# Performance work log

Hardware: AMD Instinct MI355X
Metric: run time of the kernel (lower is better)

Reference implementation:

```python
import jax, jax.numpy as jnp
import numpy as np

H_OUT, W_OUT = 473, 473  # original image size the logits are upsampled to
BN_EPS = 1e-5


def _conv(x, w, pad):
    return jax.lax.conv_general_dilated(
        x, w, window_strides=(1, 1), padding=[(pad, pad), (pad, pad)],
        dimension_numbers=('NCHW', 'OIHW', 'NCHW'))


def _bn(x, g, b):
    # BatchNorm2d in training mode: batch statistics over (N, H, W)
    m = jnp.mean(x, axis=(0, 2, 3), keepdims=True)
    v = jnp.var(x, axis=(0, 2, 3), keepdims=True)
    return (x - m) * jax.lax.rsqrt(v + BN_EPS) * g.reshape(1, -1, 1, 1) + b.reshape(1, -1, 1, 1)


def setup_inputs() -> dict:
    key = jax.random.key(0)
    ks = jax.random.split(key, 8)
    B, C, Hf, Wf, NC = 2, 256, 60, 60, 2
    return {
        'V_a': jax.random.normal(ks[0], (B, C, Hf, Wf), jnp.float32),
        'V_b': jax.random.normal(ks[1], (B, C, Hf, Wf), jnp.float32),
        'D_a': jax.random.normal(ks[2], (B, C, Hf, Wf), jnp.float32),
        'W_e': jax.random.normal(ks[3], (C, C), jnp.float32) * 0.02,
        'gate_w': jax.random.normal(ks[4], (1, C, 1, 1), jnp.float32) * 0.01,
        'conv1_w': jax.random.normal(ks[5], (C, 3 * C, 3, 3), jnp.float32) * 0.01,
        'conv2_w': jax.random.normal(ks[6], (C, 2 * C, 3, 3), jnp.float32) * 0.01,
        'bn1_g': jnp.ones((C,), jnp.float32),
        'bn1_b': jnp.zeros((C,), jnp.float32),
        'bn2_g': jnp.ones((C,), jnp.float32),
        'bn2_b': jnp.zeros((C,), jnp.float32),
        'cls1_w': jax.random.normal(ks[7], (NC, C, 1, 1), jnp.float32) * 0.01,
        'cls1_b': jnp.zeros((NC,), jnp.float32),
        'cls2_w': jax.random.normal(jax.random.fold_in(key, 9), (NC, C, 1, 1), jnp.float32) * 0.01,
        'cls2_b': jnp.zeros((NC,), jnp.float32),
    }


def reference(V_a, V_b, D_a, W_e, gate_w, conv1_w, conv2_w,
              bn1_g, bn1_b, bn2_g, bn2_b, cls1_w, cls1_b, cls2_w, cls2_b):
    B, C, Hf, Wf = V_a.shape
    N = Hf * Wf
    V_a_flat = V_a.reshape(B, C, N)
    V_b_flat = V_b.reshape(B, C, N)

    # linear_e on transposed A features, then affinity S = (A^T W^T) B
    weighted = jnp.einsum('bcn,dc->bnd', V_a_flat, W_e)        # [B, N, C]
    S = jnp.einsum('bnd,bdm->bnm', weighted, V_b_flat)         # [B, N, N]

    S_row = jax.nn.softmax(S, axis=1)                          # softmax over dim 1
    S_colT = jax.nn.softmax(jnp.swapaxes(S, 1, 2), axis=1)     # softmax of S^T over dim 1

    Z_b = jnp.einsum('bcn,bnm->bcm', V_a_flat, S_row)          # attended for view b
    Z_a = jnp.einsum('bcn,bnm->bcm', V_b_flat, S_colT)         # attended for view a

    att1 = Z_a.reshape(B, C, Hf, Wf)
    att2 = Z_b.reshape(B, C, Hf, Wf)

    # 1x1 sigmoid gates
    att1 = att1 * jax.nn.sigmoid(_conv(att1, gate_w, 0))
    att2 = att2 * jax.nn.sigmoid(_conv(att2, gate_w, 0))

    # conc1: branch-1 concatenates gated attention, RGB feat, and depth feat
    x1 = jnp.concatenate([att1, V_a, D_a], axis=1)             # [B, 3C, Hf, Wf]
    x2 = jnp.concatenate([att2, V_b], axis=1)                  # [B, 2C, Hf, Wf]

    x1 = jax.nn.relu(_bn(_conv(x1, conv1_w, 1), bn1_g, bn1_b))
    x2 = jax.nn.relu(_bn(_conv(x2, conv2_w, 1), bn2_g, bn2_b))

    x1 = _conv(x1, cls1_w, 0) + cls1_b.reshape(1, -1, 1, 1)
    x2 = _conv(x2, cls2_w, 0) + cls2_b.reshape(1, -1, 1, 1)

    NC = cls1_w.shape[0]
    x1 = jax.image.resize(x1, (B, NC, H_OUT, W_OUT), 'linear')
    x2 = jax.image.resize(x2, (B, NC, H_OUT, W_OUT), 'linear')
    return jax.nn.sigmoid(x1), jax.nn.sigmoid(x2)
```

## Files before the change

kernel.cpp:

```cpp
#include <hip/hip_runtime.h>

#define BB 2
#define CC 256
#define NN 3600
#define NCH 2
#define HO 473
#define WO 473
#define NP 3648
#define NR 3712
#define NTI 29
#define ZKS 6
#define CZKS 3

typedef unsigned short u16;
typedef __attribute__((ext_vector_type(8))) short short8;
typedef __attribute__((ext_vector_type(4))) float f32x4;

static __device__ __forceinline__ u16 f2bf(float f) {
    unsigned u = __float_as_uint(f);
    unsigned r = (u + 0x7FFF + ((u >> 16) & 1)) >> 16;
    return (u16)r;
}
static __device__ __forceinline__ u16 f2h(float f) {
    _Float16 h = (_Float16)f;
    return __builtin_bit_cast(unsigned short, h);
}
static __device__ __forceinline__ float h2f(u16 u) {
    _Float16 h = __builtin_bit_cast(_Float16, u);
    return (float)h;
}

static __device__ __forceinline__ void glds16(const u16* g, u16* l) {
    __builtin_amdgcn_global_load_lds(
        (const __attribute__((address_space(1))) void*)g,
        (__attribute__((address_space(3))) void*)l, 16, 0, 0);
}


__global__ __launch_bounds__(256)
void gemm_we(const u16* __restrict__ vat, const u16* __restrict__ web,
             u16* __restrict__ wgtb)
{
    __shared__ u16 As[128 * 64];
    __shared__ u16 Bs[128 * 64];
    const u16* A = vat + (long)blockIdx.z * NR * CC;
    u16* Cp = wgtb + (long)blockIdx.z * NR * CC;

    const int t = threadIdx.x;
    const int w = t >> 6, lane = t & 63;
    const int mh = (w >> 1) * 64, nh = (w & 1) * 64;
    const int lm = lane & 15, quad = lane >> 4;
    const int m0 = blockIdx.y * 128, n0 = blockIdx.x * 128;
    const int wb = t & 192;

    f32x4 acc[4][4] = {};

    for (int k0 = 0; k0 < CC; k0 += 64) {
#pragma unroll
        for (int i = 0; i < 4; ++i) {
            int idx = i * 256 + t;
            int row = idx >> 3;
            int sc8 = ((idx ^ row) & 7) * 8;
            glds16(A + (long)(m0 + row) * CC + k0 + sc8, &As[(i * 256 + wb) * 8]);
            glds16(web + (long)(n0 + row) * CC + k0 + sc8, &Bs[(i * 256 + wb) * 8]);
        }
        __syncthreads();
#pragma unroll
        for (int s = 0; s < 2; ++s) {
            short8 a[4], b[4];
#pragma unroll
            for (int i = 0; i < 4; ++i)
                a[i] = *(const short8*)(&As[(mh + i * 16 + lm) * 64 + ((s * 4 + quad) ^ (lm & 7)) * 8]);
#pragma unroll
            for (int j = 0; j < 4; ++j)
                b[j] = *(const short8*)(&Bs[(nh + j * 16 + lm) * 64 + ((s * 4 + quad) ^ (lm & 7)) * 8]);
#pragma unroll
            for (int i = 0; i < 4; ++i)
#pragma unroll
                for (int j = 0; j < 4; ++j)
                    acc[i][j] = __builtin_amdgcn_mfma_f32_16x16x32_bf16(a[i], b[j], acc[i][j], 0, 0, 0);
        }
        __syncthreads();
    }
#pragma unroll
    for (int i = 0; i < 4; ++i)
#pragma unroll
        for (int r = 0; r < 4; ++r) {
            int row = m0 + mh + i * 16 + quad * 4 + r;
            if (row < NN)
#pragma unroll
                for (int j = 0; j < 4; ++j) {
                    int col = n0 + nh + j * 16 + lm;
                    if (col < CC) Cp[(long)row * CC + col] = f2bf(acc[i][j][r]);
                }
        }
}

__global__ __launch_bounds__(256)
void gemm_s_stats(const u16* __restrict__ A, const u16* __restrict__ B,
                  u16* __restrict__ Sh, u16* __restrict__ STh,
                  float* __restrict__ prowm, float* __restrict__ prows,
                  float* __restrict__ pcolm, float* __restrict__ pcols)
{
    __shared__ u16 smem[17408];
    u16* As = smem;
    u16* Bs = smem + 8192;

    const int t = threadIdx.x;
    const int w = t >> 6, lane = t & 63;
    const int mh = (w >> 1) * 64, nh = (w & 1) * 64;
    const int lm = lane & 15, quad = lane >> 4;
    const int m0 = blockIdx.y * 128, n0 = blockIdx.x * 128;
    const int wb = t & 192;

    f32x4 acc[4][4] = {};

    for (int k0 = 0; k0 < CC; k0 += 64) {
#pragma unroll
        for (int i = 0; i < 4; ++i) {
            int idx = i * 256 + t;
            int row = idx >> 3;
            int sc8 = ((idx ^ row) & 7) * 8;
            glds16(A + (long)(m0 + row) * CC + k0 + sc8, &As[(i * 256 + wb) * 8]);
            glds16(B + (long)(n0 + row) * CC + k0 + sc8, &Bs[(i * 256 + wb) * 8]);
        }
        __syncthreads();
#pragma unroll
        for (int s = 0; s < 2; ++s) {
            short8 a[4], b[4];
#pragma unroll
            for (int i = 0; i < 4; ++i)
                a[i] = *(const short8*)(&As[(mh + i * 16 + lm) * 64 + ((s * 4 + quad) ^ (lm & 7)) * 8]);
#pragma unroll
            for (int j = 0; j < 4; ++j)
                b[j] = *(const short8*)(&Bs[(nh + j * 16 + lm) * 64 + ((s * 4 + quad) ^ (lm & 7)) * 8]);
#pragma unroll
            for (int i = 0; i < 4; ++i)
#pragma unroll
                for (int j = 0; j < 4; ++j)
                    acc[i][j] = __builtin_amdgcn_mfma_f32_16x16x32_bf16(a[i], b[j], acc[i][j], 0, 0, 0);
        }
        __syncthreads();
    }

#pragma unroll
    for (int i = 0; i < 4; ++i)
#pragma unroll
        for (int r = 0; r < 4; ++r) {
            int row = m0 + mh + i * 16 + quad * 4 + r;
            if (row < NN)
#pragma unroll
                for (int j = 0; j < 4; ++j) {
                    int col = n0 + nh + j * 16 + lm;
                    if (col < NN) Sh[(long)row * NP + col] = f2h(acc[i][j][r]);
                }
        }

    bool cval[4];
#pragma unroll
    for (int j = 0; j < 4; ++j) cval[j] = (n0 + nh + j * 16 + lm) < NN;

    float* sm = (float*)smem;
    float* rowm = sm;
    float* rows_ = sm + 256;
    float* colm = sm + 512;
    float* cols_ = sm + 768;
    __syncthreads();

#pragma unroll
    for (int i = 0; i < 4; ++i)
#pragma unroll
        for (int r = 0; r < 4; ++r) {
            float m = -3.0e38f;
#pragma unroll
            for (int j = 0; j < 4; ++j) if (cval[j]) m = fmaxf(m, acc[i][j][r]);
            m = fmaxf(m, __shfl_xor(m, 1, 64));
            m = fmaxf(m, __shfl_xor(m, 2, 64));
            m = fmaxf(m, __shfl_xor(m, 4, 64));
            m = fmaxf(m, __shfl_xor(m, 8, 64));
            float s = 0.f;
#pragma unroll
            for (int j = 0; j < 4; ++j) if (cval[j]) s += __expf(acc[i][j][r] - m);
            s += __shfl_xor(s, 1, 64);
            s += __shfl_xor(s, 2, 64);
            s += __shfl_xor(s, 4, 64);
            s += __shfl_xor(s, 8, 64);
            if (lm == 0) {
                int rr = mh + i * 16 + quad * 4 + r;
                rowm[(w & 1) * 128 + rr] = m;
                rows_[(w & 1) * 128 + rr] = s;
            }
        }

#pragma unroll
    for (int j = 0; j < 4; ++j) {
        float m = -3.0e38f;
#pragma unroll
        for (int i = 0; i < 4; ++i)
#pragma unroll
            for (int r = 0; r < 4; ++r)
                if (m0 + mh + i * 16 + quad * 4 + r < NN) m = fmaxf(m, acc[i][j][r]);
        m = fmaxf(m, __shfl_xor(m, 16, 64));
        m = fmaxf(m, __shfl_xor(m, 32, 64));
        float s = 0.f;
#pragma unroll
        for (int i = 0; i < 4; ++i)
#pragma unroll
            for (int r = 0; r < 4; ++r)
                if (m0 + mh + i * 16 + quad * 4 + r < NN) s += __expf(acc[i][j][r] - m);
        s += __shfl_xor(s, 16, 64);
        s += __shfl_xor(s, 32, 64);
        if (quad == 0) {
            int ccl = nh + j * 16 + lm;
            colm[(w >> 1) * 128 + ccl] = m;
            cols_[(w >> 1) * 128 + ccl] = s;
        }
    }
    __syncthreads();

    if (t < 128) {
        float m1 = rowm[t], m2 = rowm[128 + t];
        float M = fmaxf(m1, m2);
        float s = rows_[t] * __expf(m1 - M) + rows_[128 + t] * __expf(m2 - M);
        if (m0 + t < NN) {
            prowm[(long)blockIdx.x * NR + m0 + t] = M;
            prows[(long)blockIdx.x * NR + m0 + t] = s;
        }
    } else {
        int c = t - 128;
        float m1 = colm[c], m2 = colm[128 + c];
        float M = fmaxf(m1, m2);
        float s = cols_[c] * __expf(m1 - M) + cols_[128 + c] * __expf(m2 - M);
        if (n0 + c < NN) {
            pcolm[(long)blockIdx.y * NR + n0 + c] = M;
            pcols[(long)blockIdx.y * NR + n0 + c] = s;
        }
    }

    __syncthreads();
    u16* tr = smem;
#pragma unroll
    for (int i = 0; i < 4; ++i)
#pragma unroll
        for (int j = 0; j < 4; ++j)
#pragma unroll
            for (int r = 0; r < 4; ++r)
                tr[(nh + j * 16 + lm) * 136 + (mh + i * 16 + quad * 4 + r)] = f2h(acc[i][j][r]);
    __syncthreads();
    {
        int row = t >> 1, hf = t & 1;
        int mg = n0 + row;
        if (mg < NN) {
#pragma unroll
            for (int q = 0; q < 8; ++q) {
                int cb = m0 + hf * 64 + q * 8;
                if (cb < NN)
                    *(uint4*)(&STh[(long)mg * NP + cb]) =
                        *(const uint4*)(&tr[row * 136 + hf * 64 + q * 8]);
            }
        }
    }
}

__global__ __launch_bounds__(256)
void stats_combine(const float* __restrict__ prowm, const float* __restrict__ prows,
                   const float* __restrict__ pcolm, const float* __restrict__ pcols,
                   float* __restrict__ rmx, float* __restrict__ rsm,
                   float* __restrict__ cmx, float* __restrict__ csm)
{
    int i = blockIdx.x * 256 + threadIdx.x;
    if (i >= NN) return;
    const float* pm = blockIdx.y ? pcolm : prowm;
    const float* ps = blockIdx.y ? pcols : prows;
    float m = -3.0e38f, s = 0.f;
#pragma unroll 4
    for (int tI = 0; tI < NTI; ++tI) {
        float m2 = pm[(long)tI * NR + i], s2 = ps[(long)tI * NR + i];
        float M = fmaxf(m, m2);
        s = s * __expf(m - M) + s2 * __expf(m2 - M);
        m = M;
    }
    if (blockIdx.y) { cmx[i] = m; csm[i] = s; }
    else            { rmx[i] = m; rsm[i] = s; }
}

__global__ __launch_bounds__(256)
void p_build(u16* __restrict__ Sh, u16* __restrict__ STh,
             const float* __restrict__ rmx, const float* __restrict__ rsm,
             const float* __restrict__ cmx, const float* __restrict__ csm)
{
    int r = blockIdx.x;
    u16* M = blockIdx.y ? STh : Sh;
    const float* mx = blockIdx.y ? cmx : rmx;
    const float* sm = blockIdx.y ? csm : rsm;
    float mv = mx[r];
    float inv = 1.f / sm[r];
    u16* row = M + (long)r * NP;
    int t = threadIdx.x;
    for (int c0 = t * 8; c0 < NP; c0 += 2048) {
        uint4 hv = *(const uint4*)(row + c0);
        const u16* hp = (const u16*)&hv;
        u16 o[8];
#pragma unroll
        for (int e = 0; e < 8; ++e) {
            int c = c0 + e;
            o[e] = (c < NN) ? f2bf(__expf(h2f(hp[e]) - mv) * inv) : (u16)0;
        }
        *(uint4*)(row + c0) = *(const uint4*)o;
    }
}

__global__ __launch_bounds__(256, 4)
void gemm_z_128(const u16* __restrict__ vab_b, const u16* __restrict__ vbb_b,
                const u16* __restrict__ PT, const u16* __restrict__ P,
                float* __restrict__ Zb_b, float* __restrict__ Za_b)
{
    __shared__ u16 As[128 * 64];
    __shared__ u16 Bs[128 * 64];

    const int t = threadIdx.x;
    const int w = t >> 6, lane = t & 63;
    const int mh = (w >> 1) * 64, nh = (w & 1) * 64;
    const int lm = lane & 15, quad = lane >> 4;
    const int n0 = blockIdx.x * 128;
    const int ks = blockIdx.y;
    const int zz = blockIdx.z;
    const int branch = zz & 1;
    const int m0 = (zz >> 1) * 128;
    const u16* A = branch ? vbb_b : vab_b;
    const u16* B = branch ? P : PT;
    float* Cp = branch ? Za_b : Zb_b;
    const int wb = t & 192;

    const int base = 57 / ZKS, rem = 57 % ZKS;
    const int it0 = ks * base + (ks < rem ? ks : rem);
    const int itn = base + (ks < rem ? 1 : 0);

    f32x4 acc[4][4] = {};

    for (int it = it0; it < it0 + itn; ++it) {
        const int k0 = it * 64;
#pragma unroll
        for (int i = 0; i < 4; ++i) {
            int idx = i * 256 + t;
            int row = idx >> 3;
            int sc8 = ((idx ^ row) & 7) * 8;
            glds16(A + (long)(m0 + row) * NP + k0 + sc8, &As[(i * 256 + wb) * 8]);
            glds16(B + (long)(n0 + row) * NP + k0 + sc8, &Bs[(i * 256 + wb) * 8]);
        }
        __syncthreads();
#pragma unroll
        for (int s = 0; s < 2; ++s) {
            short8 a[4], b[4];
#pragma unroll
            for (int i = 0; i < 4; ++i)
                a[i] = *(const short8*)(&As[(mh + i * 16 + lm) * 64 + ((s * 4 + quad) ^ (lm & 7)) * 8]);
#pragma unroll
            for (int j = 0; j < 4; ++j)
                b[j] = *(const short8*)(&Bs[(nh + j * 16 + lm) * 64 + ((s * 4 + quad) ^ (lm & 7)) * 8]);
#pragma unroll
            for (int i = 0; i < 4; ++i)
#pragma unroll
                for (int j = 0; j < 4; ++j)
                    acc[i][j] = __builtin_amdgcn_mfma_f32_16x16x32_bf16(a[i], b[j], acc[i][j], 0, 0, 0);
        }
        __syncthreads();
    }

#pragma unroll
    for (int i = 0; i < 4; ++i)
#pragma unroll
        for (int r = 0; r < 4; ++r) {
            int row = m0 + mh + i * 16 + quad * 4 + r;
#pragma unroll
            for (int j = 0; j < 4; ++j) {
                int col = n0 + nh + j * 16 + lm;
                if (col < NN)
                    atomicAdd(&Cp[(long)row * NN + col], acc[i][j][r]);
            }
        }
}

__global__ __launch_bounds__(256, 4)
void conv_both(const u16* __restrict__ W1, const u16* __restrict__ W2,
               const u16* __restrict__ gzaT, const u16* __restrict__ vat,
               const u16* __restrict__ daT, const u16* __restrict__ gzbT,
               const u16* __restrict__ vbt, const u16* __restrict__ zbuf,
               float* __restrict__ y1, float* __restrict__ y2)
{
    __shared__ u16 As[128 * 64];
    __shared__ u16 Bs[128 * 64];

    const int t = threadIdx.x;
    const int w = t >> 6, lane = t & 63;
    const int mh = (w >> 1) * 64, nh = (w & 1) * 64;
    const int lm = lane & 15, quad = lane >> 4;
    const int wb = t & 192;

    const long L = blockIdx.x + (long)NTI * (blockIdx.y + (long)CZKS * blockIdx.z);
    const int combo = (int)(L & 7);
    const long rest = L >> 3;
    const int ks = (int)(rest % CZKS);
    const int px = (int)(rest / CZKS);
    const int which = combo >> 2;
    const int b = (combo >> 1) & 1;
    const int m0 = (combo & 1) * 128;
    const int n0 = px * 128;

    const int CIN = which ? 512 : 768;
    const int KT = 9 * CIN;
    const u16* W = which ? W2 : W1;
    const u16* P0 = which ? gzbT : gzaT;
    const u16* P1 = which ? vbt : vat;
    const u16* P2 = which ? vbt : daT;
    float* Y = which ? y2 : y1;
    const long pstride = (long)NR * CC;

    const int per = (KT / 64) / CZKS;
    const int it0 = ks * per;

    int pv[4], hv[4], wv[4], sc8v[4];
#pragma unroll
    for (int i = 0; i < 4; ++i) {
        int idx = i * 256 + t;
        int row = idx >> 3;
        sc8v[i] = ((idx ^ row) & 7) * 8;
        pv[i] = n0 + row;
        hv[i] = pv[i] / 60;
        wv[i] = pv[i] - hv[i] * 60;
    }

    f32x4 acc[4][4] = {};

    for (int it = it0; it < it0 + per; ++it) {
        const int k0 = it * 64;
        int tap = k0 / CIN;
        int kloc = k0 - tap * CIN;
        int plane = kloc >> 8, cip = kloc & 255;
        int dh = tap / 3 - 1, dw = tap - (tap / 3) * 3 - 1;
        int off = dh * 60 + dw;
        const u16* src = (plane == 0) ? P0 : ((plane == 1) ? P1 : P2);
        src += (long)b * pstride + cip;

#pragma unroll
        for (int i = 0; i < 4; ++i) {
            int idx = i * 256 + t;
            int row = idx >> 3;
            glds16(W + (long)(m0 + row) * KT + k0 + sc8v[i], &As[(i * 256 + wb) * 8]);
            bool ok = pv[i] < NN && (unsigned)(hv[i] + dh) < 60u && (unsigned)(wv[i] + dw) < 60u;
            const u16* gs = ok ? src + (long)(pv[i] + off) * CC + sc8v[i] : zbuf;
            glds16(gs, &Bs[(i * 256 + wb) * 8]);
        }
        __syncthreads();
#pragma unroll
        for (int s = 0; s < 2; ++s) {
            short8 a[4], bfr[4];
#pragma unroll
            for (int i = 0; i < 4; ++i)
                a[i] = *(const short8*)(&As[(mh + i * 16 + lm) * 64 + ((s * 4 + quad) ^ (lm & 7)) * 8]);
#pragma unroll
            for (int j = 0; j < 4; ++j)
                bfr[j] = *(const short8*)(&Bs[(nh + j * 16 + lm) * 64 + ((s * 4 + quad) ^ (lm & 7)) * 8]);
#pragma unroll
            for (int i = 0; i < 4; ++i)
#pragma unroll
                for (int j = 0; j < 4; ++j)
                    acc[i][j] = __builtin_amdgcn_mfma_f32_16x16x32_bf16(a[i], bfr[j], acc[i][j], 0, 0, 0);
        }
        __syncthreads();
    }

    float* out = Y + (long)b * CC * NN;
#pragma unroll
    for (int i = 0; i < 4; ++i)
#pragma unroll
        for (int r = 0; r < 4; ++r) {
            int row = m0 + mh + i * 16 + quad * 4 + r;
#pragma unroll
            for (int j = 0; j < 4; ++j) {
                int col = n0 + nh + j * 16 + lm;
                if (col < NN)
                    atomicAdd(&out[(long)row * NN + col], acc[i][j][r]);
            }
        }
}

__global__ __launch_bounds__(256)
void cvt_we(const float* __restrict__ W, u16* __restrict__ O)
{
    int i = blockIdx.x * 256 + threadIdx.x;
    if (i < CC * CC) O[i] = f2bf(W[i]);
}

__global__ __launch_bounds__(256)
void transpose_cvt(const float* __restrict__ V, u16* __restrict__ VT,
                   u16* __restrict__ Vpad)
{
    __shared__ float tile[64][65];
    int b = blockIdx.z, c0 = blockIdx.y * 64, n0 = blockIdx.x * 64;
    int t = threadIdx.x;
#pragma unroll
    for (int e = 0; e < 16; ++e) {
        int f = e * 256 + t; int i = f >> 6, j = f & 63;
        int n = n0 + j;
        float v = 0.f;
        if (n < NN) v = V[((long)b * CC + c0 + i) * NN + n];
        tile[i][j] = v;
        if (Vpad) Vpad[((long)b * CC + c0 + i) * NP + n] = f2bf(v);
    }
    __syncthreads();
#pragma unroll
    for (int e = 0; e < 16; ++e) {
        int f = e * 256 + t; int i = f >> 6, j = f & 63;
        int n = n0 + i;
        if (n < NN) VT[((long)b * NR + n) * CC + c0 + j] = f2bf(tile[j][i]);
    }
}

__global__ __launch_bounds__(256)
void transpose_gate(const float* __restrict__ Z, const float* __restrict__ sg,
                    u16* __restrict__ ZT)
{
    __shared__ float tile[64][65];
    int b = blockIdx.z, c0 = blockIdx.y * 64, n0 = blockIdx.x * 64;
    int t = threadIdx.x;
#pragma unroll
    for (int e = 0; e < 16; ++e) {
        int f = e * 256 + t; int i = f >> 6, j = f & 63;
        int n = n0 + j;
        float v = 0.f;
        if (n < NN) v = Z[((long)b * CC + c0 + i) * NN + n];
        tile[i][j] = v;
    }
    __syncthreads();
#pragma unroll
    for (int e = 0; e < 16; ++e) {
        int f = e * 256 + t; int i = f >> 6, j = f & 63;
        int n = n0 + i;
        if (n < NN)
            ZT[((long)b * NR + n) * CC + c0 + j] = f2bf(tile[j][i] * sg[b * NN + n]);
    }
}

template<int CIN>
__global__ __launch_bounds__(256)
void cvt_convw(const float* __restrict__ W, u16* __restrict__ O)
{
    const int KT = 9 * CIN;
    long idx = (long)blockIdx.x * 256 + threadIdx.x;
    if (idx >= (long)CC * KT) return;
    int co = (int)(idx / KT);
    int r = (int)(idx % KT);
    int tap = r / CIN, ci = r % CIN;
    O[idx] = f2bf(W[((long)co * CIN + ci) * 9 + tap]);
}

__global__ __launch_bounds__(256)
void gate_sig(const float* __restrict__ Z, const float* __restrict__ gw,
              float* __restrict__ sg)
{
    int t = threadIdx.x;
    int px = t & 63, ck = t >> 6;
    int b = blockIdx.y;
    int p = blockIdx.x * 64 + px;
    const float* Zp = Z + (long)b * CC * NN;
    float g = 0.f;
    if (p < NN) {
        for (int c = ck * 64; c < ck * 64 + 64; ++c) g += gw[c] * Zp[(long)c * NN + p];
    }
    __shared__ float red[256];
    red[t] = g;
    __syncthreads();
    if (t < 64) {
        int pp = blockIdx.x * 64 + t;
        if (pp < NN) {
            float tot = red[t] + red[t + 64] + red[t + 128] + red[t + 192];
            sg[b * NN + pp] = 1.f / (1.f + __expf(-tot));
        }
    }
}

__global__ __launch_bounds__(256)
void bn_stats_kernel(const float* __restrict__ Y, const float* __restrict__ g,
                     const float* __restrict__ beta, float* __restrict__ scale,
                     float* __restrict__ shift)
{
    int c = blockIdx.x, t = threadIdx.x;
    float s = 0.f, sq = 0.f;
    for (int b = 0; b < BB; ++b) {
        const float* p = Y + (long)b * CC * NN + (long)c * NN;
        for (int i = t; i < NN; i += 256) { float v = p[i]; s += v; sq += v * v; }
    }
    __shared__ float ls[256], lq[256];
    ls[t] = s; lq[t] = sq;
    __syncthreads();
    for (int off = 128; off > 0; off >>= 1) {
        if (t < off) { ls[t] += ls[t + off]; lq[t] += lq[t + off]; }
        __syncthreads();
    }
    if (t == 0) {
        const float inv = 1.f / (float)(BB * NN);
        float mean = ls[0] * inv;
        float var = fmaxf(lq[0] * inv - mean * mean, 0.f);
        float sc = g[c] * rsqrtf(var + 1e-5f);
        scale[c] = sc;
        shift[c] = beta[c] - mean * sc;
    }
}

__global__ __launch_bounds__(256)
void cls_kernel(const float* __restrict__ Y, const float* __restrict__ scale,
                const float* __restrict__ shift, const float* __restrict__ cw,
                const float* __restrict__ cb, float* __restrict__ O)
{
    int t = threadIdx.x;
    int px = t & 63, ck = t >> 6;
    int b = blockIdx.y;
    int p = blockIdx.x * 64 + px;
    const float* Yb = Y + (long)b * CC * NN;
    float a0 = 0.f, a1 = 0.f;
    if (p < NN) {
        for (int c = ck * 64; c < ck * 64 + 64; ++c) {
            float v = Yb[(long)c * NN + p] * scale[c] + shift[c];
            v = fmaxf(v, 0.f);
            a0 += cw[c] * v;
            a1 += cw[CC + c] * v;
        }
    }
    __shared__ float r0[256], r1[256];
    r0[t] = a0; r1[t] = a1;
    __syncthreads();
    if (t < 64) {
        int pp = blockIdx.x * 64 + t;
        if (pp < NN) {
            float s0 = r0[t] + r0[t + 64] + r0[t + 128] + r0[t + 192];
            float s1 = r1[t] + r1[t + 64] + r1[t + 128] + r1[t + 192];
            O[(long)b * NCH * NN + pp] = s0 + cb[0];
            O[(long)b * NCH * NN + NN + pp] = s1 + cb[1];
        }
    }
}

__global__ __launch_bounds__(256)
void resize_sig_kernel(const float* __restrict__ I1, const float* __restrict__ I2,
                       float* __restrict__ O)
{
    const long HALF = (long)BB * NCH * HO * WO;
    long gid = (long)blockIdx.x * 256 + threadIdx.x;
    if (gid >= HALF) return;
    int half = blockIdx.y;
    const float* I = half ? I2 : I1;
    float* Op = O + half * HALF;

    int j = (int)(gid % WO);
    long r = gid / WO;
    int i = (int)(r % HO);
    int pc = (int)(r / HO);
    const float* ip = I + (long)pc * NN;

    const float SCL = 60.0f / 473.0f;
    float fy = (i + 0.5f) * SCL - 0.5f;
    float fx = (j + 0.5f) * SCL - 0.5f;
    int y0 = (int)floorf(fy);
    int x0 = (int)floorf(fx);
    float ty = fy - (float)y0;
    float tx = fx - (float)x0;
    int y0c = max(y0, 0), y1c = min(y0 + 1, 59);
    int x0c = max(x0, 0), x1c = min(x0 + 1, 59);
    float va = ip[y0c * 60 + x0c], vb = ip[y0c * 60 + x1c];
    float vc = ip[y1c * 60 + x0c], vd = ip[y1c * 60 + x1c];
    float v = (1.f - ty) * ((1.f - tx) * va + tx * vb) + ty * ((1.f - tx) * vc + tx * vd);
    Op[gid] = 1.f / (1.f + __expf(-v));
}

extern "C" void kernel_launch(void* const* d_in, const int* in_sizes, int n_in,
                              void* d_out, int out_size, void* d_ws, size_t ws_size,
                              hipStream_t stream)
{
    const float* V_a    = (const float*)d_in[0];
    const float* V_b    = (const float*)d_in[1];
    const float* D_a    = (const float*)d_in[2];
    const float* W_e    = (const float*)d_in[3];
    const float* gate_w = (const float*)d_in[4];
    const float* conv1_w = (const float*)d_in[5];
    const float* conv2_w = (const float*)d_in[6];
    const float* bn1_g = (const float*)d_in[7];
    const float* bn1_b = (const float*)d_in[8];
    const float* bn2_g = (const float*)d_in[9];
    const float* bn2_b = (const float*)d_in[10];
    const float* cls1_w = (const float*)d_in[11];
    const float* cls1_b = (const float*)d_in[12];
    const float* cls2_w = (const float*)d_in[13];
    const float* cls2_b = (const float*)d_in[14];
    float* out = (float*)d_out;

    size_t off = 0;
    char* wsb = (char*)d_ws;
    auto carve = [&](size_t bytes) -> char* {
        char* p = wsb + off; off += (bytes + 255) & ~(size_t)255; return p;
    };

    u16* Sh    = (u16*)carve((size_t)NR * NP * 2);
    u16* STh   = (u16*)carve((size_t)NR * NP * 2);
    u16* vab   = (u16*)carve((size_t)BB * CC * NP * 2);
    u16* vbb   = (u16*)carve((size_t)BB * CC * NP * 2);
    u16* vat   = (u16*)carve((size_t)BB * NR * CC * 2);
    u16* vbt   = (u16*)carve((size_t)BB * NR * CC * 2);
    u16* daT   = (u16*)carve((size_t)BB * NR * CC * 2);
    u16* gzaT  = (u16*)carve((size_t)BB * NR * CC * 2);
    u16* gzbT  = (u16*)carve((size_t)BB * NR * CC * 2);
    u16* wgtb  = (u16*)carve((size_t)BB * NR * CC * 2);
    u16* zbuf  = (u16*)carve(256);
    u16* web   = (u16*)carve((size_t)CC * CC * 2);
    u16* wt1   = (u16*)carve((size_t)CC * 9 * 768 * 2);
    u16* wt2   = (u16*)carve((size_t)CC * 9 * 512 * 2);
    float* Za  = (float*)carve((size_t)BB * CC * NN * 4);
    float* Zb  = (float*)carve((size_t)BB * CC * NN * 4);
    float* y1  = (float*)carve((size_t)BB * CC * NN * 4);
    float* y2  = (float*)carve((size_t)BB * CC * NN * 4);
    float* rmx = (float*)carve((size_t)BB * NN * 4);
    float* rsm = (float*)carve((size_t)BB * NN * 4);
    float* cmx = (float*)carve((size_t)BB * NN * 4);
    float* csm = (float*)carve((size_t)BB * NN * 4);
    float* sga = (float*)carve((size_t)BB * NN * 4);
    float* sgb = (float*)carve((size_t)BB * NN * 4);
    float* prm = (float*)carve((size_t)NTI * NR * 4);
    float* prs = (float*)carve((size_t)NTI * NR * 4);
    float* pcm = (float*)carve((size_t)NTI * NR * 4);
    float* pcs = (float*)carve((size_t)NTI * NR * 4);
    float* c1o = (float*)carve((size_t)BB * NCH * NN * 4);
    float* c2o = (float*)carve((size_t)BB * NCH * NN * 4);

    dim3 blk(256);

    hipMemsetAsync(Za, 0, (size_t)4 * BB * CC * NN * 4, stream);
    hipMemsetAsync(vat, 0, (size_t)6 * ((size_t)BB * NR * CC * 2) + 256, stream);

    cvt_we<<<256, blk, 0, stream>>>(W_e, web);
    transpose_cvt<<<dim3(57, 4, BB), blk, 0, stream>>>(V_a, vat, vab);
    transpose_cvt<<<dim3(57, 4, BB), blk, 0, stream>>>(V_b, vbt, vbb);
    transpose_cvt<<<dim3(57, 4, BB), blk, 0, stream>>>(D_a, daT, nullptr);
    cvt_convw<768><<<(int)(((long)CC * 9 * 768 + 255) / 256), blk, 0, stream>>>(conv1_w, wt1);
    cvt_convw<512><<<(int)(((long)CC * 9 * 512 + 255) / 256), blk, 0, stream>>>(conv2_w, wt2);

    gemm_we<<<dim3(2, NTI, BB), blk, 0, stream>>>(vat, web, wgtb);

    for (int b = 0; b < BB; ++b) {
        const u16* wgtb_b = wgtb + (long)b * NR * CC;
        const u16* vbt_b  = vbt + (long)b * NR * CC;
        const u16* vab_b  = vab + (long)b * CC * NP;
        const u16* vbb_b  = vbb + (long)b * CC * NP;
        float* rmx_b = rmx + b * NN; float* rsm_b = rsm + b * NN;
        float* cmx_b = cmx + b * NN; float* csm_b = csm + b * NN;

        gemm_s_stats<<<dim3(NTI, NTI), blk, 0, stream>>>(
            wgtb_b, vbt_b, Sh, STh, prm, prs, pcm, pcs);
        stats_combine<<<dim3((NN + 255) / 256, 2), blk, 0, stream>>>(
            prm, prs, pcm, pcs, rmx_b, rsm_b, cmx_b, csm_b);
        p_build<<<dim3(NN, 2), blk, 0, stream>>>(Sh, STh, rmx_b, rsm_b, cmx_b, csm_b);
        gemm_z_128<<<dim3(NTI, ZKS, 4), blk, 0, stream>>>(
            vab_b, vbb_b, STh, Sh,
            Zb + (long)b * CC * NN, Za + (long)b * CC * NN);
    }

    gate_sig<<<dim3(57, BB), blk, 0, stream>>>(Za, gate_w, sga);
    gate_sig<<<dim3(57, BB), blk, 0, stream>>>(Zb, gate_w, sgb);
    transpose_gate<<<dim3(57, 4, BB), blk, 0, stream>>>(Za, sga, gzaT);
    transpose_gate<<<dim3(57, 4, BB), blk, 0, stream>>>(Zb, sgb, gzbT);

    conv_both<<<dim3(NTI, CZKS, 8), blk, 0, stream>>>(
        wt1, wt2, gzaT, vat, daT, gzbT, vbt, zbuf, y1, y2);

    bn_stats_kernel<<<256, blk, 0, stream>>>(y1, bn1_g, bn1_b, rmx, rsm);
    bn_stats_kernel<<<256, blk, 0, stream>>>(y2, bn2_g, bn2_b, cmx, csm);
    cls_kernel<<<dim3(57, BB), blk, 0, stream>>>(y1, rmx, rsm, cls1_w, cls1_b, c1o);
    cls_kernel<<<dim3(57, BB), blk, 0, stream>>>(y2, cmx, csm, cls2_w, cls2_b, c2o);

    resize_sig_kernel<<<dim3((int)(((long)BB * NCH * HO * WO + 255) / 256), 2), blk, 0, stream>>>(c1o, c2o, out);
}
```

Before: 597.4 us.

## Batch paired kernels, fold stats combine into p_build, coalesce S stores, reorder conv K

```diff
diff --git a/kernel.cpp b/kernel.cpp
--- a/kernel.cpp
+++ b/kernel.cpp
@@ -143,18 +143,30 @@
         __syncthreads();
     }
 
+    u16* tr = smem;
+
 #pragma unroll
     for (int i = 0; i < 4; ++i)
 #pragma unroll
-        for (int r = 0; r < 4; ++r) {
-            int row = m0 + mh + i * 16 + quad * 4 + r;
-            if (row < NN)
-#pragma unroll
-                for (int j = 0; j < 4; ++j) {
-                    int col = n0 + nh + j * 16 + lm;
-                    if (col < NN) Sh[(long)row * NP + col] = f2h(acc[i][j][r]);
-                }
-        }
+        for (int j = 0; j < 4; ++j)
+#pragma unroll
+            for (int r = 0; r < 4; ++r)
+                tr[(mh + i * 16 + quad * 4 + r) * 136 + (nh + j * 16 + lm)] = f2h(acc[i][j][r]);
+    __syncthreads();
+    {
+        int row = t >> 1, hf = t & 1;
+        int ng = m0 + row;
+        if (ng < NN) {
+#pragma unroll
+            for (int q = 0; q < 8; ++q) {
+                int cb = n0 + hf * 64 + q * 8;
+                if (cb < NN)
+                    *(uint4*)(&Sh[(long)ng * NP + cb]) =
+                        *(const uint4*)(&tr[row * 136 + hf * 64 + q * 8]);
+            }
+        }
+    }
+    __syncthreads();
 
     bool cval[4];
 #pragma unroll
@@ -165,7 +177,6 @@
     float* rows_ = sm + 256;
     float* colm = sm + 512;
     float* cols_ = sm + 768;
-    __syncthreads();
 
 #pragma unroll
     for (int i = 0; i < 4; ++i)
@@ -238,7 +249,6 @@
     }
 
     __syncthreads();
-    u16* tr = smem;
 #pragma unroll
     for (int i = 0; i < 4; ++i)
 #pragma unroll
@@ -263,38 +273,23 @@
 }
 
 __global__ __launch_bounds__(256)
-void stats_combine(const float* __restrict__ prowm, const float* __restrict__ prows,
-                   const float* __restrict__ pcolm, const float* __restrict__ pcols,
-                   float* __restrict__ rmx, float* __restrict__ rsm,
-                   float* __restrict__ cmx, float* __restrict__ csm)
-{
-    int i = blockIdx.x * 256 + threadIdx.x;
-    if (i >= NN) return;
-    const float* pm = blockIdx.y ? pcolm : prowm;
-    const float* ps = blockIdx.y ? pcols : prows;
+void p_build(u16* __restrict__ Sh, u16* __restrict__ STh,
+             const float* __restrict__ prm, const float* __restrict__ prs,
+             const float* __restrict__ pcm, const float* __restrict__ pcs)
+{
+    int r = blockIdx.x;
+    u16* M = blockIdx.y ? STh : Sh;
+    const float* pm = blockIdx.y ? pcm : prm;
+    const float* ps = blockIdx.y ? pcs : prs;
     float m = -3.0e38f, s = 0.f;
 #pragma unroll 4
     for (int tI = 0; tI < NTI; ++tI) {
-        float m2 = pm[(long)tI * NR + i], s2 = ps[(long)tI * NR + i];
-        float M = fmaxf(m, m2);
-        s = s * __expf(m - M) + s2 * __expf(m2 - M);
-        m = M;
-    }
-    if (blockIdx.y) { cmx[i] = m; csm[i] = s; }
-    else            { rmx[i] = m; rsm[i] = s; }
-}
-
-__global__ __launch_bounds__(256)
-void p_build(u16* __restrict__ Sh, u16* __restrict__ STh,
-             const float* __restrict__ rmx, const float* __restrict__ rsm,
-             const float* __restrict__ cmx, const float* __restrict__ csm)
-{
-    int r = blockIdx.x;
-    u16* M = blockIdx.y ? STh : Sh;
-    const float* mx = blockIdx.y ? cmx : rmx;
-    const float* sm = blockIdx.y ? csm : rsm;
-    float mv = mx[r];
-    float inv = 1.f / sm[r];
+        float m2 = pm[(long)tI * NR + r], s2 = ps[(long)tI * NR + r];
+        float M2 = fmaxf(m, m2);
+        s = s * __expf(m - M2) + s2 * __expf(m2 - M2);
+        m = M2;
+    }
+    float inv = 1.f / s;
     u16* row = M + (long)r * NP;
     int t = threadIdx.x;
     for (int c0 = t * 8; c0 < NP; c0 += 2048) {
@@ -304,7 +299,7 @@
 #pragma unroll
         for (int e = 0; e < 8; ++e) {
             int c = c0 + e;
-            o[e] = (c < NN) ? f2bf(__expf(h2f(hp[e]) - mv) * inv) : (u16)0;
+            o[e] = (c < NN) ? f2bf(__expf(h2f(hp[e]) - m) * inv) : (u16)0;
         }
         *(uint4*)(row + c0) = *(const uint4*)o;
     }
@@ -416,39 +411,43 @@
     float* Y = which ? y2 : y1;
     const long pstride = (long)NR * CC;
 
-    const int per = (KT / 64) / CZKS;
-    const int it0 = ks * per;
-
-    int pv[4], hv[4], wv[4], sc8v[4];
+    const int PER = 3 * (CIN / 64);
+    const int it0 = ks * PER;
+    const int dh = ks - 1;
+
+    int rowv[4], sc8v[4], rb[4];
+    bool okd[4][3];
 #pragma unroll
     for (int i = 0; i < 4; ++i) {
         int idx = i * 256 + t;
         int row = idx >> 3;
+        rowv[i] = row;
         sc8v[i] = ((idx ^ row) & 7) * 8;
-        pv[i] = n0 + row;
-        hv[i] = pv[i] / 60;
-        wv[i] = pv[i] - hv[i] * 60;
+        int p = n0 + row;
+        int h = p / 60, wp = p - h * 60;
+        rb[i] = (p + dh * 60) * CC + sc8v[i];
+        bool hok = (p < NN) && ((unsigned)(h + dh) < 60u);
+#pragma unroll
+        for (int d = 0; d < 3; ++d)
+            okd[i][d] = hok && ((unsigned)(wp + d - 1) < 60u);
     }
 
     f32x4 acc[4][4] = {};
 
-    for (int it = it0; it < it0 + per; ++it) {
+    for (int it = it0; it < it0 + PER; ++it) {
         const int k0 = it * 64;
-        int tap = k0 / CIN;
-        int kloc = k0 - tap * CIN;
-        int plane = kloc >> 8, cip = kloc & 255;
-        int dh = tap / 3 - 1, dw = tap - (tap / 3) * 3 - 1;
-        int off = dh * 60 + dw;
-        const u16* src = (plane == 0) ? P0 : ((plane == 1) ? P1 : P2);
-        src += (long)b * pstride + cip;
+        const int g = it - it0;
+        const int dw = g % 3;
+        const int pc = g / 3;
+        const int plane = pc >> 2;
+        const int cip = (pc & 3) * 64;
+        const u16* srcp = ((plane == 0) ? P0 : (plane == 1) ? P1 : P2)
+                          + (long)b * pstride + cip;
 
 #pragma unroll
         for (int i = 0; i < 4; ++i) {
-            int idx = i * 256 + t;
-            int row = idx >> 3;
-            glds16(W + (long)(m0 + row) * KT + k0 + sc8v[i], &As[(i * 256 + wb) * 8]);
-            bool ok = pv[i] < NN && (unsigned)(hv[i] + dh) < 60u && (unsigned)(wv[i] + dw) < 60u;
-            const u16* gs = ok ? src + (long)(pv[i] + off) * CC + sc8v[i] : zbuf;
+            glds16(W + (long)(m0 + rowv[i]) * KT + k0 + sc8v[i], &As[(i * 256 + wb) * 8]);
+            const u16* gs = okd[i][dw] ? srcp + rb[i] + (dw - 1) * CC : zbuf;
             glds16(gs, &Bs[(i * 256 + wb) * 8]);
         }
         __syncthreads();
@@ -493,11 +492,20 @@
 }
 
 __global__ __launch_bounds__(256)
-void transpose_cvt(const float* __restrict__ V, u16* __restrict__ VT,
-                   u16* __restrict__ Vpad)
+void transpose_cvt3(const float* __restrict__ Va, const float* __restrict__ Vb,
+                    const float* __restrict__ Da,
+                    u16* __restrict__ vat, u16* __restrict__ vbt,
+                    u16* __restrict__ daT,
+                    u16* __restrict__ vab, u16* __restrict__ vbb)
 {
     __shared__ float tile[64][65];
-    int b = blockIdx.z, c0 = blockIdx.y * 64, n0 = blockIdx.x * 64;
+    int z = blockIdx.z;
+    int s = z % 3, b = z / 3;
+    const float* V = (s == 0) ? Va : (s == 1) ? Vb : Da;
+    u16* VT = (s == 0) ? vat : (s == 1) ? vbt : daT;
+    u16* Vpad = (s == 0) ? vab : (s == 1) ? vbb : nullptr;
+
+    int c0 = blockIdx.y * 64, n0 = blockIdx.x * 64;
     int t = threadIdx.x;
 #pragma unroll
     for (int e = 0; e < 16; ++e) {
@@ -518,11 +526,18 @@
 }
 
 __global__ __launch_bounds__(256)
-void transpose_gate(const float* __restrict__ Z, const float* __restrict__ sg,
-                    u16* __restrict__ ZT)
+void transpose_gate(const float* __restrict__ Za, const float* __restrict__ Zb,
+                    const float* __restrict__ sga, const float* __restrict__ sgb,
+                    u16* __restrict__ gzaT, u16* __restrict__ gzbT)
 {
     __shared__ float tile[64][65];
-    int b = blockIdx.z, c0 = blockIdx.y * 64, n0 = blockIdx.x * 64;
+    int z = blockIdx.z;
+    int b = z & 1, ab = z >> 1;
+    const float* Z = ab ? Zb : Za;
+    const float* sg = ab ? sgb : sga;
+    u16* ZT = ab ? gzbT : gzaT;
+
+    int c0 = blockIdx.y * 64, n0 = blockIdx.x * 64;
     int t = threadIdx.x;
 #pragma unroll
     for (int e = 0; e < 16; ++e) {
@@ -547,21 +562,30 @@
 void cvt_convw(const float* __restrict__ W, u16* __restrict__ O)
 {
     const int KT = 9 * CIN;
+    const int PER = 3 * (CIN / 64);
     long idx = (long)blockIdx.x * 256 + threadIdx.x;
     if (idx >= (long)CC * KT) return;
     int co = (int)(idx / KT);
     int r = (int)(idx % KT);
-    int tap = r / CIN, ci = r % CIN;
+    int c64 = r >> 6, within = r & 63;
+    int ks = c64 / PER, g = c64 % PER;
+    int dw = g % 3, pc = g / 3;
+    int tap = ks * 3 + dw;
+    int ci = pc * 64 + within;
     O[idx] = f2bf(W[((long)co * CIN + ci) * 9 + tap]);
 }
 
 __global__ __launch_bounds__(256)
-void gate_sig(const float* __restrict__ Z, const float* __restrict__ gw,
-              float* __restrict__ sg)
+void gate_sig(const float* __restrict__ Za, const float* __restrict__ Zb,
+              const float* __restrict__ gw,
+              float* __restrict__ sga, float* __restrict__ sgb)
 {
     int t = threadIdx.x;
     int px = t & 63, ck = t >> 6;
     int b = blockIdx.y;
+    int ab = blockIdx.z;
+    const float* Z = ab ? Zb : Za;
+    float* sg = ab ? sgb : sga;
     int p = blockIdx.x * 64 + px;
     const float* Zp = Z + (long)b * CC * NN;
     float g = 0.f;
@@ -581,11 +605,19 @@
 }
 
 __global__ __launch_bounds__(256)
-void bn_stats_kernel(const float* __restrict__ Y, const float* __restrict__ g,
-                     const float* __restrict__ beta, float* __restrict__ scale,
-                     float* __restrict__ shift)
-{
-    int c = blockIdx.x, t = threadIdx.x;
+void bn_stats_kernel(const float* __restrict__ y1, const float* __restrict__ y2,
+                     const float* __restrict__ g1, const float* __restrict__ b1,
+                     const float* __restrict__ g2, const float* __restrict__ b2,
+                     float* __restrict__ sc1, float* __restrict__ sh1,
+                     float* __restrict__ sc2, float* __restrict__ sh2)
+{
+    int which = blockIdx.x >> 8;
+    int c = blockIdx.x & 255, t = threadIdx.x;
+    const float* Y = which ? y2 : y1;
+    const float* g = which ? g2 : g1;
+    const float* beta = which ? b2 : b1;
+    float* scale = which ? sc2 : sc1;
+    float* shift = which ? sh2 : sh1;
     float s = 0.f, sq = 0.f;
     for (int b = 0; b < BB; ++b) {
         const float* p = Y + (long)b * CC * NN + (long)c * NN;
@@ -609,10 +641,21 @@
 }
 
 __global__ __launch_bounds__(256)
-void cls_kernel(const float* __restrict__ Y, const float* __restrict__ scale,
-                const float* __restrict__ shift, const float* __restrict__ cw,
-                const float* __restrict__ cb, float* __restrict__ O)
-{
+void cls_kernel(const float* __restrict__ y1, const float* __restrict__ y2,
+                const float* __restrict__ sc1, const float* __restrict__ sh1,
+                const float* __restrict__ sc2, const float* __restrict__ sh2,
+                const float* __restrict__ cw1, const float* __restrict__ cb1,
+                const float* __restrict__ cw2, const float* __restrict__ cb2,
+                float* __restrict__ O1, float* __restrict__ O2)
+{
+    int which = blockIdx.z;
+    const float* Y = which ? y2 : y1;
+    const float* scale = which ? sc2 : sc1;
+    const float* shift = which ? sh2 : sh1;
+    const float* cw = which ? cw2 : cw1;
+    const float* cb = which ? cb2 : cb1;
+    float* O = which ? O2 : O1;
+
     int t = threadIdx.x;
     int px = t & 63, ck = t >> 6;
     int b = blockIdx.y;
@@ -737,9 +780,8 @@
     hipMemsetAsync(vat, 0, (size_t)6 * ((size_t)BB * NR * CC * 2) + 256, stream);
 
     cvt_we<<<256, blk, 0, stream>>>(W_e, web);
-    transpose_cvt<<<dim3(57, 4, BB), blk, 0, stream>>>(V_a, vat, vab);
-    transpose_cvt<<<dim3(57, 4, BB), blk, 0, stream>>>(V_b, vbt, vbb);
-    transpose_cvt<<<dim3(57, 4, BB), blk, 0, stream>>>(D_a, daT, nullptr);
+    transpose_cvt3<<<dim3(57, 4, 3 * BB), blk, 0, stream>>>(
+        V_a, V_b, D_a, vat, vbt, daT, vab, vbb);
     cvt_convw<768><<<(int)(((long)CC * 9 * 768 + 255) / 256), blk, 0, stream>>>(conv1_w, wt1);
     cvt_convw<512><<<(int)(((long)CC * 9 * 512 + 255) / 256), blk, 0, stream>>>(conv2_w, wt2);
 
@@ -750,31 +792,25 @@
         const u16* vbt_b  = vbt + (long)b * NR * CC;
         const u16* vab_b  = vab + (long)b * CC * NP;
         const u16* vbb_b  = vbb + (long)b * CC * NP;
-        float* rmx_b = rmx + b * NN; float* rsm_b = rsm + b * NN;
-        float* cmx_b = cmx + b * NN; float* csm_b = csm + b * NN;
 
         gemm_s_stats<<<dim3(NTI, NTI), blk, 0, stream>>>(
             wgtb_b, vbt_b, Sh, STh, prm, prs, pcm, pcs);
-        stats_combine<<<dim3((NN + 255) / 256, 2), blk, 0, stream>>>(
-            prm, prs, pcm, pcs, rmx_b, rsm_b, cmx_b, csm_b);
-        p_build<<<dim3(NN, 2), blk, 0, stream>>>(Sh, STh, rmx_b, rsm_b, cmx_b, csm_b);
+        p_build<<<dim3(NN, 2), blk, 0, stream>>>(Sh, STh, prm, prs, pcm, pcs);
         gemm_z_128<<<dim3(NTI, ZKS, 4), blk, 0, stream>>>(
             vab_b, vbb_b, STh, Sh,
             Zb + (long)b * CC * NN, Za + (long)b * CC * NN);
     }
 
-    gate_sig<<<dim3(57, BB), blk, 0, stream>>>(Za, gate_w, sga);
-    gate_sig<<<dim3(57, BB), blk, 0, stream>>>(Zb, gate_w, sgb);
-    transpose_gate<<<dim3(57, 4, BB), blk, 0, stream>>>(Za, sga, gzaT);
-    transpose_gate<<<dim3(57, 4, BB), blk, 0, stream>>>(Zb, sgb, gzbT);
+    gate_sig<<<dim3(57, BB, 2), blk, 0, stream>>>(Za, Zb, gate_w, sga, sgb);
+    transpose_gate<<<dim3(57, 4, 2 * BB), blk, 0, stream>>>(Za, Zb, sga, sgb, gzaT, gzbT);
 
     conv_both<<<dim3(NTI, CZKS, 8), blk, 0, stream>>>(
         wt1, wt2, gzaT, vat, daT, gzbT, vbt, zbuf, y1, y2);
 
-    bn_stats_kernel<<<256, blk, 0, stream>>>(y1, bn1_g, bn1_b, rmx, rsm);
-    bn_stats_kernel<<<256, blk, 0, stream>>>(y2, bn2_g, bn2_b, cmx, csm);
-    cls_kernel<<<dim3(57, BB), blk, 0, stream>>>(y1, rmx, rsm, cls1_w, cls1_b, c1o);
-    cls_kernel<<<dim3(57, BB), blk, 0, stream>>>(y2, cmx, csm, cls2_w, cls2_b, c2o);
+    bn_stats_kernel<<<2 * CC, blk, 0, stream>>>(
+        y1, y2, bn1_g, bn1_b, bn2_g, bn2_b, rmx, rsm, cmx, csm);
+    cls_kernel<<<dim3(57, BB, 2), blk, 0, stream>>>(
+        y1, y2, rmx, rsm, cmx, csm, cls1_w, cls1_b, cls2_w, cls2_b, c1o, c2o);
 
     resize_sig_kernel<<<dim3((int)(((long)BB * NCH * HO * WO + 255) / 256), 2), blk, 0, stream>>>(c1o, c2o, out);
 }
```

Measured after the change: 594.7 us. No clear change (-0.5%).
